# Kernel optimization log

Measured on AMD Instinct MI355X. Metric: run time of the kernel, lower is better.

## Reference

```python
import jax, jax.numpy as jnp
import numpy as np

WS = 7          # window size
NH = 12         # num heads
DIM = 384
HID = 4 * DIM
EPS = 1e-5


def _rel_pos_index(ws):
    coords = np.stack(np.meshgrid(np.arange(ws), np.arange(ws), indexing='ij'))  # (2,ws,ws)
    cf = coords.reshape(2, -1)
    rel = cf[:, :, None] - cf[:, None, :]           # (2,N,N)
    rel = rel.transpose(1, 2, 0)                    # (N,N,2)
    rel[:, :, 0] += ws - 1
    rel[:, :, 1] += ws - 1
    rel[:, :, 0] *= 2 * ws - 1
    return jnp.asarray(rel.sum(-1))                 # (N,N) int

REL_IDX = _rel_pos_index(WS)


def _layernorm(x, g, b):
    m = x.mean(-1, keepdims=True)
    v = ((x - m) ** 2).mean(-1, keepdims=True)
    return (x - m) * jax.lax.rsqrt(v + EPS) * g + b


def setup_inputs() -> dict:
    key = jax.random.key(0)
    ks = jax.random.split(key, 16)
    B, H, W = 8, 112, 112
    s = lambda fan: 1.0 / np.sqrt(fan)
    return {
        'x': jax.random.normal(ks[0], (B, DIM, H, W), jnp.float32),
        'g1': jnp.ones((DIM,), jnp.float32),
        'b1': jnp.zeros((DIM,), jnp.float32),
        'w_qkv': jax.random.normal(ks[1], (DIM, 3 * DIM), jnp.float32) * s(DIM),
        'b_qkv': jnp.zeros((3 * DIM,), jnp.float32),
        'rpb': jax.random.normal(ks[2], ((2 * WS - 1) ** 2, NH), jnp.float32) * 0.02,
        'w_proj': jax.random.normal(ks[3], (DIM, DIM), jnp.float32) * s(DIM),
        'b_proj': jnp.zeros((DIM,), jnp.float32),
        'g2': jnp.ones((DIM,), jnp.float32),
        'b2': jnp.zeros((DIM,), jnp.float32),
        'w_fc1': jax.random.normal(ks[4], (DIM, HID), jnp.float32) * s(DIM),
        'b_fc1': jnp.zeros((HID,), jnp.float32),
        'w_fc2': jax.random.normal(ks[5], (HID, DIM), jnp.float32) * s(HID),
        'b_fc2': jnp.zeros((DIM,), jnp.float32),
    }


def reference(x, g1, b1, w_qkv, b_qkv, rpb, w_proj, b_proj, g2, b2, w_fc1, b_fc1, w_fc2, b_fc2):
    B, C, H, W = x.shape
    x = x.transpose(0, 2, 3, 1)                     # (B,H,W,C)
    shortcut = x
    xn = _layernorm(x, g1, b1)

    # window partition (with padding, no-op when divisible)
    pad_h = (-H) % WS
    pad_w = (-W) % WS
    if pad_h or pad_w:
        xn = jnp.pad(xn, ((0, 0), (0, pad_h), (0, pad_w), (0, 0)))
    Hp, Wp = H + pad_h, W + pad_w
    N = WS * WS
    xw = xn.reshape(B, Hp // WS, WS, Wp // WS, WS, C).transpose(0, 1, 3, 2, 4, 5)
    xw = xw.reshape(-1, N, C)                       # (B_, N, C)
    B_ = xw.shape[0]
    hd = C // NH

    qkv = (xw @ w_qkv + b_qkv).reshape(B_, N, 3, NH, hd)
    q = qkv[:, :, 0].transpose(0, 2, 1, 3) * (hd ** -0.5)   # (B_,h,N,d)
    k = qkv[:, :, 1].transpose(0, 2, 1, 3)
    v = qkv[:, :, 2].transpose(0, 2, 1, 3)

    attn = jnp.einsum('bhnd,bhmd->bhnm', q, k)
    bias = rpb[REL_IDX.reshape(-1)].reshape(N, N, NH).transpose(2, 0, 1)  # (h,N,N)
    attn = jax.nn.softmax(attn + bias[None], axis=-1)

    out = jnp.einsum('bhnm,bhmd->bhnd', attn, v).transpose(0, 2, 1, 3).reshape(B_, N, C)
    out = out @ w_proj + b_proj

    # window reverse
    out = out.reshape(B, Hp // WS, Wp // WS, WS, WS, C).transpose(0, 1, 3, 2, 4, 5)
    out = out.reshape(B, Hp, Wp, C)[:, :H, :W]

    x = shortcut + out
    h = _layernorm(x, g2, b2)
    h = jax.nn.gelu(h @ w_fc1 + b_fc1, approximate=False) @ w_fc2 + b_fc2
    x = x + h
    return x.transpose(0, 3, 1, 2)                  # (B,C,H,W)
```

## Files before the change

kernel.cpp:

```cpp
#include <hip/hip_runtime.h>
#include <cstdint>
#include <cmath>

using u16 = unsigned short;

typedef __bf16 bf16x8 __attribute__((ext_vector_type(8)));
typedef float  f32x4  __attribute__((ext_vector_type(4)));

__device__ __forceinline__ float b2f(u16 u) {
    return __uint_as_float(((unsigned int)u) << 16);
}
__device__ __forceinline__ u16 f2b(float f) {
    unsigned int x = __float_as_uint(f);
    unsigned int r = (x + 0x7fffu + ((x >> 16) & 1u)) >> 16;
    return (u16)r;
}

__device__ __forceinline__ void gload16(const u16* g, u16* l) {
    __builtin_amdgcn_global_load_lds((__attribute__((address_space(1))) void*)g,
                                     (__attribute__((address_space(3))) void*)l,
                                     16, 0, 0);
}

#define LGKM0_FENCE() do { \
    asm volatile("s_waitcnt lgkmcnt(0)" ::: "memory"); \
    __builtin_amdgcn_sched_barrier(0); } while (0)

__device__ __forceinline__ float gelu_f(float x) {
    float z = fabsf(x) * 0.70710678118f;
    float t = __builtin_amdgcn_rcpf(fmaf(0.3275911f, z, 1.0f));
    float poly = fmaf(fmaf(fmaf(fmaf(1.061405429f, t, -1.453152027f),
                               t, 1.421413741f),
                          t, -0.284496736f),
                     t, 0.254829592f) * t;
    float e = __expf(-z * z);
    float erfv = copysignf(1.0f - poly * e, x);
    return 0.5f * x * (1.0f + erfv);
}

__device__ __forceinline__ int tprime(int b, int hw) {
    int r = hw / 112, c = hw - r * 112;
    int wy = r / 7, iy = r - wy * 7;
    int wx = c / 7, ix = c - wx * 7;
    return (b * 256 + wy * 16 + wx) * 49 + iy * 7 + ix;
}

__global__ void detect_dtype(const unsigned int* __restrict__ x, int* __restrict__ flag) {
    __shared__ int cnt[256];
    int tid = threadIdx.x;
    int c = 0;
#pragma unroll
    for (int i = 0; i < 16; ++i) {
        unsigned int w = x[tid * 16 + i];
        int e = (w >> 23) & 0xFF;
        if (e >= 100 && e <= 150) ++c;
    }
    cnt[tid] = c;
    __syncthreads();
    if (tid == 0) {
        int s = 0;
        for (int i = 0; i < 256; ++i) s += cnt[i];
        flag[0] = (s > 3072) ? 1 : 0;
    }
}

__global__ void convertk(const void* __restrict__ src, u16* __restrict__ dst, int n,
                         const int* __restrict__ flagp) {
    int isf = flagp[0];
    int i = blockIdx.x * 256 + threadIdx.x;
    if (i < n) dst[i] = isf ? f2b(((const float*)src)[i]) : ((const u16*)src)[i];
}

__global__ void wtrans(const u16* __restrict__ in, u16* __restrict__ out, int K, int N) {
    __shared__ u16 tile[32][33];
    int n0 = blockIdx.x * 32, k0 = blockIdx.y * 32;
    int tx = threadIdx.x & 31, ty = threadIdx.x >> 5;
#pragma unroll
    for (int i = 0; i < 4; ++i)
        tile[ty + i * 8][tx] = in[(size_t)(k0 + ty + i * 8) * N + n0 + tx];
    __syncthreads();
#pragma unroll
    for (int i = 0; i < 4; ++i)
        out[(size_t)(n0 + ty + i * 8) * K + k0 + tx] = tile[tx][ty + i * 8];
}

__global__ void ln1_stats(const void* __restrict__ x, float* __restrict__ mean,
                          float* __restrict__ rstd, const int* __restrict__ flagp) {
    int isf = flagp[0];
    int t = blockIdx.x * 256 + threadIdx.x;
    int b = t / 12544, hw = t - b * 12544;
    size_t base = (size_t)b * 384 * 12544 + hw;
    float s = 0.f, sq = 0.f;
    if (isf) {
        const float* p = (const float*)x + base;
        for (int c = 0; c < 384; ++c) {
            float v = p[(size_t)c * 12544];
            s += v; sq += v * v;
        }
    } else {
        const u16* p = (const u16*)x + base;
        for (int c = 0; c < 384; ++c) {
            float v = b2f(p[(size_t)c * 12544]);
            s += v; sq += v * v;
        }
    }
    float m = s * (1.0f / 384.0f);
    float var = sq * (1.0f / 384.0f) - m * m;
    mean[t] = m;
    rstd[t] = rsqrtf(var + 1e-5f);
}

__global__ void ln1_apply(const void* __restrict__ x, const float* __restrict__ mean,
                          const float* __restrict__ rstd, const u16* __restrict__ g1,
                          const u16* __restrict__ b1, u16* __restrict__ xt,
                          u16* __restrict__ xn, const int* __restrict__ flagp) {
    __shared__ float tile[64][65];
    int isf = flagp[0];
    int hw0 = blockIdx.x * 64, c0 = blockIdx.y * 64, b = blockIdx.z;
    int tid = threadIdx.x;
    {
        int hl = tid & 63, cq = tid >> 6;
        size_t base = ((size_t)b * 384 + c0) * 12544 + hw0;
#pragma unroll
        for (int it = 0; it < 16; ++it) {
            int cl = cq * 16 + it;
            size_t idx = base + (size_t)cl * 12544 + hl;
            tile[cl][hl] = isf ? ((const float*)x)[idx] : b2f(((const u16*)x)[idx]);
        }
    }
    __syncthreads();
    {
        int cl = tid & 63, hq = tid >> 6;
        float g = b2f(g1[c0 + cl]), bb = b2f(b1[c0 + cl]);
#pragma unroll
        for (int it = 0; it < 16; ++it) {
            int hl = hq * 16 + it;
            int hw = hw0 + hl;
            int t = b * 12544 + hw;
            int tp = tprime(b, hw);
            float v = tile[cl][hl];
            size_t o = (size_t)tp * 384 + c0 + cl;
            xt[o] = f2b(v);
            xn[o] = f2b((v - mean[t]) * rstd[t] * g + bb);
        }
    }
}

template <int EPI>
__global__ void gemm_bt(const u16* __restrict__ A, const u16* __restrict__ Bt,
                        const u16* __restrict__ bias, const u16* __restrict__ res,
                        u16* __restrict__ Cout, int M, int N, int K) {
    __shared__ __align__(16) u16 S[2][2][128 * 32];
    const int tid = threadIdx.x;
    const int wave = tid >> 6, lane = tid & 63;

    const int nbx = gridDim.x;
    const int nwg = nbx * gridDim.y;
    int flat = blockIdx.y * nbx + blockIdx.x;
    {
        int q = nwg >> 3, r = nwg & 7;
        int xcd = flat & 7, loc = flat >> 3;
        flat = (xcd < r ? xcd * (q + 1) : r * (q + 1) + (xcd - r) * q) + loc;
    }
    const int m0 = (flat / nbx) * 128, n0 = (flat % nbx) * 128;

    const int wm = wave & 1, wn = wave >> 1;
    const int m15 = lane & 15, q4 = lane >> 4;

    const u16* gA = A + (size_t)(m0 + wave * 32 + (lane >> 2)) * K + (lane & 3) * 8;
    const u16* gB = Bt + (size_t)(n0 + wave * 32 + (lane >> 2)) * K + (lane & 3) * 8;

    f32x4 acc[4][4];
#pragma unroll
    for (int i = 0; i < 4; ++i)
#pragma unroll
        for (int j = 0; j < 4; ++j) acc[i][j] = {0.f, 0.f, 0.f, 0.f};

    const int nt = K >> 5;
    {
        u16* lA = &S[0][0][(wave * 32) * 32];
        u16* lB = &S[0][1][(wave * 32) * 32];
        gload16(gA, lA);
        gload16(gA + 16 * (size_t)K, lA + 16 * 32);
        gload16(gB, lB);
        gload16(gB + 16 * (size_t)K, lB + 16 * 32);
    }
    __syncthreads();

    for (int t = 0; t < nt; ++t) {
        const int cur = t & 1;
        if (t + 1 < nt) {
            const int k0 = (t + 1) << 5;
            u16* lA = &S[cur ^ 1][0][(wave * 32) * 32];
            u16* lB = &S[cur ^ 1][1][(wave * 32) * 32];
            gload16(gA + k0, lA);
            gload16(gA + k0 + 16 * (size_t)K, lA + 16 * 32);
            gload16(gB + k0, lB);
            gload16(gB + k0 + 16 * (size_t)K, lB + 16 * 32);
        }
        bf16x8 af[4], bfr[4];
#pragma unroll
        for (int i = 0; i < 4; ++i)
            af[i] = *(const bf16x8*)&S[cur][0][(wm * 64 + i * 16 + m15) * 32 + q4 * 8];
#pragma unroll
        for (int j = 0; j < 4; ++j)
            bfr[j] = *(const bf16x8*)&S[cur][1][(wn * 64 + j * 16 + m15) * 32 + q4 * 8];
#pragma unroll
        for (int i = 0; i < 4; ++i)
#pragma unroll
            for (int j = 0; j < 4; ++j)
                acc[i][j] = __builtin_amdgcn_mfma_f32_16x16x32_bf16(af[i], bfr[j],
                                                                    acc[i][j], 0, 0, 0);
        __syncthreads();
    }

    constexpr int CSTR = 132;
    float* Cs = (float*)&S[0][0][0];
#pragma unroll
    for (int p = 0; p < 4; ++p) {
        __syncthreads();
        if (wm == (p >> 1)) {
            const int ibase = (p & 1) * 2;
#pragma unroll
            for (int jj = 0; jj < 4; ++jj) {
                int n = n0 + wn * 64 + jj * 16 + m15;
                float bv = b2f(bias[n]);
#pragma unroll
                for (int ii = 0; ii < 2; ++ii) {
                    int i = ibase + ii;
#pragma unroll
                    for (int r = 0; r < 4; ++r) {
                        float v = acc[i][jj][r] + bv;
                        if (EPI == 1) v = gelu_f(v);
                        Cs[(ii * 16 + q4 * 4 + r) * CSTR + wn * 64 + jj * 16 + m15] = v;
                    }
                }
            }
        }
        __syncthreads();
#pragma unroll
        for (int it = 0; it < 2; ++it) {
            int r2 = it * 16 + (tid >> 4);
            int c8 = (tid & 15) * 8;
            size_t goff = (size_t)(m0 + p * 32 + r2) * N + n0 + c8;
            f32x4 v0 = *(const f32x4*)&Cs[r2 * CSTR + c8];
            f32x4 v1 = *(const f32x4*)&Cs[r2 * CSTR + c8 + 4];
            uint4 rv = {0u, 0u, 0u, 0u};
            const u16* rp = (const u16*)&rv;
            if (EPI == 2) rv = *(const uint4*)&res[goff];
            u16 outv[8];
#pragma unroll
            for (int e = 0; e < 4; ++e) {
                float a = v0[e];
                if (EPI == 2) a += b2f(rp[e]);
                outv[e] = f2b(a);
                float bq = v1[e];
                if (EPI == 2) bq += b2f(rp[4 + e]);
                outv[4 + e] = f2b(bq);
            }
            *(uint4*)&Cout[goff] = *(const uint4*)outv;
        }
    }
}

__global__ __launch_bounds__(256, 4)
void attn_win(const u16* __restrict__ qkv, const u16* __restrict__ rpb,
              u16* __restrict__ outp) {
    __shared__ __align__(16) u16 lds[4][4096];
    const int tid = threadIdx.x;
    const int wave = tid >> 6, lane = tid & 63;
    const int t0p = blockIdx.x * 49;
    u16* Vt = &lds[wave][0];
    u16* Ps = &lds[wave][0];
    u16* Po = &lds[wave][0];
    const int m15 = lane & 15, q4 = lane >> 4;
    const int rr = lane >> 2, dq = lane & 3;
    const float scale = 0.17677669529663687f;

    for (int hl = 0; hl < 3; ++hl) {
        const int h = hl * 4 + wave;
        const u16* qbase = qkv + (size_t)t0p * 1152 + h * 32;
        bf16x8 qf[4], kf[4];
#pragma unroll
        for (int i = 0; i < 4; ++i) {
            int row = i * 16 + m15;
            int rc = row < 49 ? row : 48;
            const u16* g = qbase + (size_t)rc * 1152 + q4 * 8;
            qf[i] = *(const bf16x8*)g;
            kf[i] = *(const bf16x8*)(g + 384);
        }
#pragma unroll
        for (int p = 0; p < 4; ++p) {
            int n = p * 16 + rr;
            uint4 vv = {0u, 0u, 0u, 0u};
            if (n < 49)
                vv = *(const uint4*)(qbase + (size_t)n * 1152 + 768 + dq * 8);
            const u16* pv = (const u16*)&vv;
#pragma unroll
            for (int ii = 0; ii < 8; ++ii) Vt[(dq * 8 + ii) * 64 + n] = pv[ii];
        }
        LGKM0_FENCE();
        bf16x8 vf[2][2];
#pragma unroll
        for (int j = 0; j < 2; ++j)
#pragma unroll
            for (int kk = 0; kk < 2; ++kk)
                vf[j][kk] = *(const bf16x8*)&Vt[(j * 16 + m15) * 64 + kk * 32 + q4 * 8];
        f32x4 sc[4][4];
#pragma unroll
        for (int i = 0; i < 4; ++i)
#pragma unroll
            for (int j = 0; j < 4; ++j) {
                sc[i][j] = {0.f, 0.f, 0.f, 0.f};
                sc[i][j] = __builtin_amdgcn_mfma_f32_16x16x32_bf16(qf[i], kf[j],
                                                                   sc[i][j], 0, 0, 0);
            }
#pragma unroll
        for (int i = 0; i < 4; ++i) {
#pragma unroll
            for (int r = 0; r < 4; ++r) {
                int row = i * 16 + q4 * 4 + r;
                int rc = row < 49 ? row : 48;
                int ri = rc / 7, rj = rc - ri * 7;
#pragma unroll
                for (int j = 0; j < 4; ++j) {
                    int col = j * 16 + m15;
                    int cc = col < 49 ? col : 48;
                    int mi = cc / 7, mj = cc - mi * 7;
                    int idx = ((ri - mi + 6) * 13 + (rj - mj + 6)) * 12 + h;
                    float bias = b2f(rpb[idx]);
                    float s = sc[i][j][r] * scale + bias;
                    sc[i][j][r] = (row < 49 && col < 49) ? s : -1e30f;
                }
            }
        }
#pragma unroll
        for (int i = 0; i < 4; ++i) {
#pragma unroll
            for (int r = 0; r < 4; ++r) {
                float mx = fmaxf(fmaxf(sc[i][0][r], sc[i][1][r]),
                                 fmaxf(sc[i][2][r], sc[i][3][r]));
                mx = fmaxf(mx, __shfl_xor(mx, 1));
                mx = fmaxf(mx, __shfl_xor(mx, 2));
                mx = fmaxf(mx, __shfl_xor(mx, 4));
                mx = fmaxf(mx, __shfl_xor(mx, 8));
                float e0 = __expf(sc[i][0][r] - mx);
                float e1 = __expf(sc[i][1][r] - mx);
                float e2 = __expf(sc[i][2][r] - mx);
                float e3 = __expf(sc[i][3][r] - mx);
                float sum = e0 + e1 + e2 + e3;
                sum += __shfl_xor(sum, 1);
                sum += __shfl_xor(sum, 2);
                sum += __shfl_xor(sum, 4);
                sum += __shfl_xor(sum, 8);
                float inv = 1.0f / sum;
                sc[i][0][r] = e0 * inv;
                sc[i][1][r] = e1 * inv;
                sc[i][2][r] = e2 * inv;
                sc[i][3][r] = e3 * inv;
            }
        }
#pragma unroll
        for (int i = 0; i < 4; ++i)
#pragma unroll
            for (int r = 0; r < 4; ++r)
#pragma unroll
                for (int j = 0; j < 4; ++j)
                    Ps[(i * 16 + q4 * 4 + r) * 64 + j * 16 + m15] = f2b(sc[i][j][r]);
        LGKM0_FENCE();
        f32x4 oacc[4][2];
#pragma unroll
        for (int i = 0; i < 4; ++i)
#pragma unroll
            for (int j = 0; j < 2; ++j) oacc[i][j] = {0.f, 0.f, 0.f, 0.f};
#pragma unroll
        for (int i = 0; i < 4; ++i) {
#pragma unroll
            for (int kk = 0; kk < 2; ++kk) {
                bf16x8 pf = *(const bf16x8*)&Ps[(i * 16 + m15) * 64 + kk * 32 + q4 * 8];
#pragma unroll
                for (int j = 0; j < 2; ++j)
                    oacc[i][j] = __builtin_amdgcn_mfma_f32_16x16x32_bf16(pf, vf[j][kk],
                                                                         oacc[i][j], 0, 0, 0);
            }
        }
#pragma unroll
        for (int i = 0; i < 4; ++i)
#pragma unroll
            for (int r = 0; r < 4; ++r) {
                int row = i * 16 + q4 * 4 + r;
#pragma unroll
                for (int j = 0; j < 2; ++j)
                    Po[row * 40 + j * 16 + m15] = f2b(oacc[i][j][r]);
            }
        LGKM0_FENCE();
#pragma unroll
        for (int w2 = 0; w2 < 4; ++w2) {
            int row = w2 * 16 + rr;
            if (row < 49) {
                uint4 ov = *(const uint4*)&Po[row * 40 + dq * 8];
                *(uint4*)&outp[(size_t)(t0p + row) * 384 + h * 32 + dq * 8] = ov;
            }
        }
    }
}

__global__ void ln2_kernel(const u16* __restrict__ y, const u16* __restrict__ g2,
                           const u16* __restrict__ b2, u16* __restrict__ out) {
    int wave = threadIdx.x >> 6, lane = threadIdx.x & 63;
    size_t t = (size_t)blockIdx.x * 4 + wave;
    const u16* row = y + t * 384;
    float v[6];
    float s = 0.f, sq = 0.f;
#pragma unroll
    for (int i = 0; i < 6; ++i) {
        v[i] = b2f(row[lane + i * 64]);
        s += v[i]; sq += v[i] * v[i];
    }
#pragma unroll
    for (int m = 1; m < 64; m <<= 1) {
        s += __shfl_xor(s, m);
        sq += __shfl_xor(sq, m);
    }
    float mean = s * (1.0f / 384.0f);
    float var = sq * (1.0f / 384.0f) - mean * mean;
    float rstd = rsqrtf(var + 1e-5f);
#pragma unroll
    for (int i = 0; i < 6; ++i) {
        int c = lane + i * 64;
        out[t * 384 + c] = f2b((v[i] - mean) * rstd * b2f(g2[c]) + b2f(b2[c]));
    }
}

__global__ void out_transpose(const u16* __restrict__ fin, void* __restrict__ out,
                              const int* __restrict__ flagp) {
    __shared__ float tile[64][65];
    int isf = flagp[0];
    int hw0 = blockIdx.x * 64, c0 = blockIdx.y * 64, b = blockIdx.z;
    int tid = threadIdx.x;
    {
        int cl = tid & 63, hq = tid >> 6;
#pragma unroll
        for (int it = 0; it < 16; ++it) {
            int hl = hq * 16 + it;
            int tp = tprime(b, hw0 + hl);
            tile[hl][cl] = b2f(fin[(size_t)tp * 384 + c0 + cl]);
        }
    }
    __syncthreads();
    {
        int hl = tid & 63, cq = tid >> 6;
#pragma unroll
        for (int it = 0; it < 16; ++it) {
            int cl = cq * 16 + it;
            size_t o = ((size_t)b * 384 + c0 + cl) * 12544 + hw0 + hl;
            float v = tile[hl][cl];
            if (isf) ((float*)out)[o] = v;
            else     ((u16*)out)[o] = f2b(v);
        }
    }
}

extern "C" void kernel_launch(void* const* d_in, const int* in_sizes, int n_in,
                              void* d_out, int out_size, void* d_ws, size_t ws_size,
                              hipStream_t stream) {
    constexpr int T = 100352, C = 384, HID = 1536, NQ = 1152;
    const void* x      = d_in[0];
    u16* out_any = (u16*)d_out;
    (void)out_any;

    char* ws = (char*)d_ws;
    size_t off = 0;
    auto alloc = [&](size_t bytes) { char* p = ws + off; off += (bytes + 255) & ~(size_t)255; return p; };
    int*   flag   = (int*)alloc(4);
    u16* cw_qkv  = (u16*)alloc((size_t)C * NQ * 2);
    u16* cb_qkv  = (u16*)alloc((size_t)NQ * 2);
    u16* crpb    = (u16*)alloc((size_t)169 * 12 * 2);
    u16* cw_proj = (u16*)alloc((size_t)C * C * 2);
    u16* cb_proj = (u16*)alloc((size_t)C * 2);
    u16* cg1     = (u16*)alloc((size_t)C * 2);
    u16* cb1     = (u16*)alloc((size_t)C * 2);
    u16* cg2     = (u16*)alloc((size_t)C * 2);
    u16* cb2     = (u16*)alloc((size_t)C * 2);
    u16* cw_fc1  = (u16*)alloc((size_t)C * HID * 2);
    u16* cb_fc1  = (u16*)alloc((size_t)HID * 2);
    u16* cw_fc2  = (u16*)alloc((size_t)HID * C * 2);
    u16* cb_fc2  = (u16*)alloc((size_t)C * 2);
    u16* wqkvT  = (u16*)alloc((size_t)C * NQ * 2);
    u16* wprojT = (u16*)alloc((size_t)C * C * 2);
    u16* wfc1T  = (u16*)alloc((size_t)C * HID * 2);
    u16* wfc2T  = (u16*)alloc((size_t)HID * C * 2);
    u16*   xt     = (u16*)alloc((size_t)T * C * 2);
    u16*   bufB   = (u16*)alloc((size_t)T * C * 2);
    u16*   bufC   = (u16*)alloc((size_t)T * HID * 2);
    u16*   ybuf   = (u16*)alloc((size_t)T * C * 2);
    float* meanb  = (float*)alloc((size_t)T * 4);
    float* rstdb  = (float*)alloc((size_t)T * 4);

    detect_dtype<<<1, 256, 0, stream>>>((const unsigned int*)x, flag);

    auto conv = [&](const void* src, u16* dst, int n) {
        convertk<<<(n + 255) / 256, 256, 0, stream>>>(src, dst, n, flag);
    };
    conv(d_in[1], cg1, C);
    conv(d_in[2], cb1, C);
    conv(d_in[3], cw_qkv, C * NQ);
    conv(d_in[4], cb_qkv, NQ);
    conv(d_in[5], crpb, 169 * 12);
    conv(d_in[6], cw_proj, C * C);
    conv(d_in[7], cb_proj, C);
    conv(d_in[8], cg2, C);
    conv(d_in[9], cb2, C);
    conv(d_in[10], cw_fc1, C * HID);
    conv(d_in[11], cb_fc1, HID);
    conv(d_in[12], cw_fc2, HID * C);
    conv(d_in[13], cb_fc2, C);

    wtrans<<<dim3(NQ / 32, C / 32), 256, 0, stream>>>(cw_qkv, wqkvT, C, NQ);
    wtrans<<<dim3(C / 32, C / 32), 256, 0, stream>>>(cw_proj, wprojT, C, C);
    wtrans<<<dim3(HID / 32, C / 32), 256, 0, stream>>>(cw_fc1, wfc1T, C, HID);
    wtrans<<<dim3(C / 32, HID / 32), 256, 0, stream>>>(cw_fc2, wfc2T, HID, C);

    ln1_stats<<<T / 256, 256, 0, stream>>>(x, meanb, rstdb, flag);
    ln1_apply<<<dim3(196, 6, 8), 256, 0, stream>>>(x, meanb, rstdb, cg1, cb1, xt, bufB, flag);

    gemm_bt<0><<<dim3(NQ / 128, T / 128), 256, 0, stream>>>(bufB, wqkvT, cb_qkv, nullptr,
                                                            bufC, T, NQ, C);
    attn_win<<<2048, 256, 0, stream>>>(bufC, crpb, bufB);

    gemm_bt<2><<<dim3(C / 128, T / 128), 256, 0, stream>>>(bufB, wprojT, cb_proj, xt,
                                                           ybuf, T, C, C);
    ln2_kernel<<<T / 4, 256, 0, stream>>>(ybuf, cg2, cb2, bufB);

    gemm_bt<1><<<dim3(HID / 128, T / 128), 256, 0, stream>>>(bufB, wfc1T, cb_fc1, nullptr,
                                                             bufC, T, HID, C);
    gemm_bt<2><<<dim3(C / 128, T / 128), 256, 0, stream>>>(bufC, wfc2T, cb_fc2, ybuf,
                                                           bufB, T, C, HID);
    out_transpose<<<dim3(196, 6, 8), 256, 0, stream>>>(bufB, d_out, flag);
}
```

Baseline: 1.338 ms.

## Precompute expanded relative-position bias and prefetch next head's QKV in attention

Adds a small kernel that expands the relative position bias table into a dense per-head 64x64 float matrix with -1e30 masking, so the attention kernel does one load and fma per score instead of index arithmetic, a gather and masking. The attention head loop is unrolled and software-pipelined: Q, K and V for the next head are loaded into registers while the current head is computed. Launch bounds drop from 4 to 3 blocks per SM to make room for the extra registers, which lowers occupancy, and the bias reads become fp32 global loads.

```diff
diff --git a/kernel.cpp b/kernel.cpp
--- a/kernel.cpp
+++ b/kernel.cpp
@@ -69,6 +69,18 @@
     int isf = flagp[0];
     int i = blockIdx.x * 256 + threadIdx.x;
     if (i < n) dst[i] = isf ? f2b(((const float*)src)[i]) : ((const u16*)src)[i];
+}
+
+__global__ void build_bias(const u16* __restrict__ crpb, float* __restrict__ bias_exp) {
+    int row = blockIdx.x, h = blockIdx.y, col = threadIdx.x;
+    float v = -1e30f;
+    if (row < 49 && col < 49) {
+        int ri = row / 7, rj = row - ri * 7;
+        int mi = col / 7, mj = col - mi * 7;
+        int idx = ((ri - mi + 6) * 13 + (rj - mj + 6)) * 12 + h;
+        v = b2f(crpb[idx]);
+    }
+    bias_exp[(h * 64 + row) * 64 + col] = v;
 }
 
 __global__ void wtrans(const u16* __restrict__ in, u16* __restrict__ out, int K, int N) {
@@ -263,8 +275,8 @@
     }
 }
 
-__global__ __launch_bounds__(256, 4)
-void attn_win(const u16* __restrict__ qkv, const u16* __restrict__ rpb,
+__global__ __launch_bounds__(256, 3)
+void attn_win(const u16* __restrict__ qkv, const float* __restrict__ bias_exp,
               u16* __restrict__ outp) {
     __shared__ __align__(16) u16 lds[4][4096];
     const int tid = threadIdx.x;
@@ -276,28 +288,48 @@
     const int m15 = lane & 15, q4 = lane >> 4;
     const int rr = lane >> 2, dq = lane & 3;
     const float scale = 0.17677669529663687f;
-
-    for (int hl = 0; hl < 3; ++hl) {
-        const int h = hl * 4 + wave;
-        const u16* qbase = qkv + (size_t)t0p * 1152 + h * 32;
-        bf16x8 qf[4], kf[4];
+    const u16* wbase = qkv + (size_t)t0p * 1152;
+
+    auto loadQK = [&](int h, bf16x8* qf, bf16x8* kf) {
 #pragma unroll
         for (int i = 0; i < 4; ++i) {
             int row = i * 16 + m15;
             int rc = row < 49 ? row : 48;
-            const u16* g = qbase + (size_t)rc * 1152 + q4 * 8;
+            const u16* g = wbase + (size_t)rc * 1152 + h * 32 + q4 * 8;
             qf[i] = *(const bf16x8*)g;
             kf[i] = *(const bf16x8*)(g + 384);
         }
+    };
+    auto loadV = [&](int h, uint4* vv) {
 #pragma unroll
         for (int p = 0; p < 4; ++p) {
             int n = p * 16 + rr;
-            uint4 vv = {0u, 0u, 0u, 0u};
+            vv[p] = {0u, 0u, 0u, 0u};
             if (n < 49)
-                vv = *(const uint4*)(qbase + (size_t)n * 1152 + 768 + dq * 8);
-            const u16* pv = (const u16*)&vv;
+                vv[p] = *(const uint4*)(wbase + (size_t)n * 1152 + 768 + h * 32 + dq * 8);
+        }
+    };
+
+    bf16x8 qfA[4], kfA[4];
+    uint4 vvA[4];
+    loadQK(wave, qfA, kfA);
+    loadV(wave, vvA);
+
+#pragma unroll
+    for (int hl = 0; hl < 3; ++hl) {
+        const int h = hl * 4 + wave;
+#pragma unroll
+        for (int p = 0; p < 4; ++p) {
+            int n = p * 16 + rr;
+            const u16* pv = (const u16*)&vvA[p];
 #pragma unroll
             for (int ii = 0; ii < 8; ++ii) Vt[(dq * 8 + ii) * 64 + n] = pv[ii];
+        }
+        bf16x8 qfB[4], kfB[4];
+        uint4 vvB[4];
+        if (hl < 2) {
+            loadQK(h + 4, qfB, kfB);
+            loadV(h + 4, vvB);
         }
         LGKM0_FENCE();
         bf16x8 vf[2][2];
@@ -312,28 +344,19 @@
 #pragma unroll
             for (int j = 0; j < 4; ++j) {
                 sc[i][j] = {0.f, 0.f, 0.f, 0.f};
-                sc[i][j] = __builtin_amdgcn_mfma_f32_16x16x32_bf16(qf[i], kf[j],
+                sc[i][j] = __builtin_amdgcn_mfma_f32_16x16x32_bf16(qfA[i], kfA[j],
                                                                    sc[i][j], 0, 0, 0);
             }
-#pragma unroll
-        for (int i = 0; i < 4; ++i) {
+        const float* bx = bias_exp + h * 4096;
+#pragma unroll
+        for (int i = 0; i < 4; ++i)
 #pragma unroll
             for (int r = 0; r < 4; ++r) {
                 int row = i * 16 + q4 * 4 + r;
-                int rc = row < 49 ? row : 48;
-                int ri = rc / 7, rj = rc - ri * 7;
-#pragma unroll
-                for (int j = 0; j < 4; ++j) {
-                    int col = j * 16 + m15;
-                    int cc = col < 49 ? col : 48;
-                    int mi = cc / 7, mj = cc - mi * 7;
-                    int idx = ((ri - mi + 6) * 13 + (rj - mj + 6)) * 12 + h;
-                    float bias = b2f(rpb[idx]);
-                    float s = sc[i][j][r] * scale + bias;
-                    sc[i][j][r] = (row < 49 && col < 49) ? s : -1e30f;
-                }
-            }
-        }
+#pragma unroll
+                for (int j = 0; j < 4; ++j)
+                    sc[i][j][r] = fmaf(sc[i][j][r], scale, bx[row * 64 + j * 16 + m15]);
+            }
 #pragma unroll
         for (int i = 0; i < 4; ++i) {
 #pragma unroll
@@ -402,6 +425,14 @@
                 *(uint4*)&outp[(size_t)(t0p + row) * 384 + h * 32 + dq * 8] = ov;
             }
         }
+        if (hl < 2) {
+#pragma unroll
+            for (int i = 0; i < 4; ++i) {
+                qfA[i] = qfB[i];
+                kfA[i] = kfB[i];
+                vvA[i] = vvB[i];
+            }
+        }
     }
 }
 
@@ -490,6 +521,7 @@
     u16* wprojT = (u16*)alloc((size_t)C * C * 2);
     u16* wfc1T  = (u16*)alloc((size_t)C * HID * 2);
     u16* wfc2T  = (u16*)alloc((size_t)HID * C * 2);
+    float* biasx = (float*)alloc((size_t)12 * 64 * 64 * 4);
     u16*   xt     = (u16*)alloc((size_t)T * C * 2);
     u16*   bufB   = (u16*)alloc((size_t)T * C * 2);
     u16*   bufC   = (u16*)alloc((size_t)T * HID * 2);
@@ -516,6 +548,8 @@
     conv(d_in[12], cw_fc2, HID * C);
     conv(d_in[13], cb_fc2, C);
 
+    build_bias<<<dim3(64, 12), 64, 0, stream>>>(crpb, biasx);
+
     wtrans<<<dim3(NQ / 32, C / 32), 256, 0, stream>>>(cw_qkv, wqkvT, C, NQ);
     wtrans<<<dim3(C / 32, C / 32), 256, 0, stream>>>(cw_proj, wprojT, C, C);
     wtrans<<<dim3(HID / 32, C / 32), 256, 0, stream>>>(cw_fc1, wfc1T, C, HID);
@@ -526,7 +560,7 @@
 
     gemm_bt<0><<<dim3(NQ / 128, T / 128), 256, 0, stream>>>(bufB, wqkvT, cb_qkv, nullptr,
                                                             bufC, T, NQ, C);
-    attn_win<<<2048, 256, 0, stream>>>(bufC, crpb, bufB);
+    attn_win<<<2048, 256, 0, stream>>>(bufC, biasx, bufB);
 
     gemm_bt<2><<<dim3(C / 128, T / 128), 256, 0, stream>>>(bufB, wprojT, cb_proj, xt,
                                                            ybuf, T, C, C);
```

Result: faster. 1.281 ms (-4.3%).
